# Performance work log

Measured on AMD Instinct MI355X. Metric: run time of the kernel, lower is better.

The kernel has to match this reference:

```python
import jax, jax.numpy as jnp
import numpy as np

B, F, C, O, M = 128, 4096, 32, 32, 9  # batch, num_fields, in_ch, out_ch, num_coeffs (moves incl. self)


def setup_inputs() -> dict:
    key = jax.random.key(0)
    k1, k2, k3, k4 = jax.random.split(key, 4)
    x = jax.random.normal(k1, (B, F, C), dtype=jnp.float32)
    # mask[m, f] = index of the source field feeding target field f via move m
    mask = jax.random.randint(k2, (M, F), 0, F, dtype=jnp.int32)
    init_std = 1.0 / (3.0 * np.sqrt(C * O))  # matches TruncatedNormal stddev in build()
    conv_coeffs = jax.random.normal(k3, (M, C, O), dtype=jnp.float32) * init_std
    # biases are zero-initialized in the original; use small random values so the
    # bias-add path is exercised numerically
    biases = jax.random.normal(k4, (F, O), dtype=jnp.float32) * 0.01
    return {"x": x, "mask": mask, "conv_coeffs": conv_coeffs, "biases": biases}


def reference(x, mask, conv_coeffs, biases):
    # ch_convolve_by_moves: gather source fields per move, per-move matmul, per-field bias.
    # gathered[b, m, f, c] = x[b, mask[m, f], c]
    gathered = jnp.take(x, mask, axis=1)              # [B, M, F, C]
    out = jnp.einsum('bmfc,mco->bfo', gathered, conv_coeffs)  # sum over moves and in-channels
    return out + biases                               # per-field bias broadcast over batch
```

## Files before the change

kernel.cpp:

```cpp
#include <hip/hip_runtime.h>


#define B_ 128
#define F_ 4096
#define C_ 32
#define O_ 32
#define M_ 9
#define T_ 18
#define TF1 32
#define LROW1 528

typedef _Float16 halfx4 __attribute__((ext_vector_type(4)));
typedef _Float16 halfx8 __attribute__((ext_vector_type(8)));
typedef float floatx4 __attribute__((ext_vector_type(4)));
typedef float floatx16 __attribute__((ext_vector_type(16)));

__global__ __launch_bounds__(256) void pass1_transpose(
    const float* __restrict__ x, const float* __restrict__ coeffs,
    _Float16* __restrict__ xh, _Float16* __restrict__ wf)
{
    __shared__ _Float16 tile[TF1 * LROW1];
    const int blk = blockIdx.x;
    const int bs  = blk & 7;
    const int f0  = (blk >> 3) * TF1;
    const int tid = threadIdx.x;

    {
        const int f_l = tid >> 3;
        const int c4  = (tid & 7) * 4;
        const float* src = x + ((size_t)f0 + f_l) * C_ + c4;
#pragma unroll
        for (int bp = 0; bp < 16; ++bp) {
            const floatx4* p = reinterpret_cast<const floatx4*>(
                src + (size_t)(bs * 16 + bp) * (F_ * C_));
            floatx4 v = __builtin_nontemporal_load(p);
            halfx4 hv;
            hv[0] = (_Float16)v[0]; hv[1] = (_Float16)v[1];
            hv[2] = (_Float16)v[2]; hv[3] = (_Float16)v[3];
            *reinterpret_cast<halfx4*>(&tile[f_l * LROW1 + bp * C_ + c4]) = hv;
        }
    }
    __syncthreads();

    {
        const int wv   = tid >> 6;
        const int lane = tid & 63;
#pragma unroll
        for (int it = 0; it < TF1 / 4; ++it) {
            int f_l = it * 4 + wv;
            halfx8 v = *reinterpret_cast<const halfx8*>(&tile[f_l * LROW1 + lane * 8]);
            *reinterpret_cast<halfx8*>(
                xh + ((size_t)bs * F_ + f0 + f_l) * (16 * C_) + lane * 8) = v;
        }
    }

    if (blk == 0) {
        for (int id = tid; id < T_ * 64; id += 256) {
            int t  = id >> 6;
            int L  = id & 63;
            int m  = t >> 1;
            int cb = 16 * (t & 1) + 8 * (L >> 5);
            int o  = L & 31;
            halfx8 w;
#pragma unroll
            for (int j = 0; j < 8; ++j)
                w[j] = (_Float16)coeffs[(m * C_ + cb + j) * O_ + o];
            *reinterpret_cast<halfx8*>(wf + id * 8) = w;
        }
    }
}

__global__ __launch_bounds__(256, 4) void pass2_gemm(
    const _Float16* __restrict__ xh, const _Float16* __restrict__ wf,
    const int* __restrict__ mask, const float* __restrict__ biases,
    float* __restrict__ out)
{
    __shared__ _Float16 sw[T_ * 64 * 8];
    const int tid = threadIdx.x;
#pragma unroll
    for (int i = tid; i < T_ * 64; i += 256)
        reinterpret_cast<halfx8*>(sw)[i] = reinterpret_cast<const halfx8*>(wf)[i];
    __syncthreads();

    const int blk  = blockIdx.x;
    const int bs   = blk & 7;
    const int fg   = blk >> 3;
    const int wave = tid >> 6;
    const int lane = tid & 63;
    const int h    = lane >> 5;
    const int row  = lane & 31;
    const int fi   = row >> 4;
    const int bp   = row & 15;
    const int ocol = lane & 31;

    const int fa = fg * 8 + 2 * wave;
    const int f  = fa + fi;

    const _Float16* xb = xh + (size_t)bs * F_ * (16 * C_) + bp * C_ + 8 * h;

    int sidx[M_];
#pragma unroll
    for (int m = 0; m < M_; ++m) sidx[m] = mask[m * F_ + f];

    halfx8 a[T_];
#pragma unroll
    for (int m = 0; m < M_; ++m) {
        const _Float16* rp = xb + (size_t)sidx[m] * (16 * C_);
        a[2 * m]     = *reinterpret_cast<const halfx8*>(rp);
        a[2 * m + 1] = *reinterpret_cast<const halfx8*>(rp + 16);
    }

    floatx16 acc;
#pragma unroll
    for (int i = 0; i < 16; ++i) acc[i] = 0.0f;
#pragma unroll
    for (int t = 0; t < T_; ++t) {
        halfx8 bwt = *reinterpret_cast<const halfx8*>(&sw[(t * 64 + lane) * 8]);
        acc = __builtin_amdgcn_mfma_f32_32x32x16_f16(a[t], bwt, acc, 0, 0, 0);
    }

    float bias_a = biases[(size_t)fa * O_ + ocol];
    float bias_b = biases[(size_t)(fa + 1) * O_ + ocol];
#pragma unroll
    for (int r = 0; r < 16; ++r) {
        int orow = (r & 3) + 8 * (r >> 2) + 4 * h;
        int ofi  = orow >> 4;
        int b    = bs * 16 + (orow & 15);
        float v  = acc[r] + (ofi ? bias_b : bias_a);
        __builtin_nontemporal_store(
            v, &out[((size_t)b * F_ + fa + ofi) * O_ + ocol]);
    }
}

__global__ __launch_bounds__(256) void fallback_kernel(
    const float* __restrict__ x, const int* __restrict__ mask,
    const float* __restrict__ coeffs, const float* __restrict__ biases,
    float* __restrict__ out)
{
    int gid = blockIdx.x * 256 + threadIdx.x;
    int o = gid & (O_ - 1);
    int f = (gid >> 5) & (F_ - 1);
    int b = gid >> 17;
    float acc = biases[f * O_ + o];
    for (int m = 0; m < M_; ++m) {
        int s = mask[m * F_ + f];
        const float* xr = x + ((size_t)b * F_ + s) * C_;
        const float* wr = coeffs + (m * C_) * O_ + o;
#pragma unroll
        for (int c = 0; c < C_; ++c)
            acc += xr[c] * wr[c * O_];
    }
    out[gid] = acc;
}

extern "C" void kernel_launch(void* const* d_in, const int* in_sizes, int n_in,
                              void* d_out, int out_size, void* d_ws, size_t ws_size,
                              hipStream_t stream) {
    const float* x      = (const float*)d_in[0];
    const int*   mask   = (const int*)d_in[1];
    const float* coeffs = (const float*)d_in[2];
    const float* biases = (const float*)d_in[3];
    float* out = (float*)d_out;

    const size_t xh_elems = (size_t)B_ * F_ * C_;
    const size_t need = xh_elems * sizeof(_Float16) + (size_t)T_ * 64 * 8 * sizeof(_Float16);

    if (ws_size >= need) {
        _Float16* xh = (_Float16*)d_ws;
        _Float16* wf = xh + xh_elems;
        pass1_transpose<<<8 * (F_ / TF1), 256, 0, stream>>>(x, coeffs, xh, wf);
        pass2_gemm<<<8 * (F_ / 8), 256, 0, stream>>>(xh, wf, mask, biases, out);
    } else {
        fallback_kernel<<<(B_ * F_ * O_) / 256, 256, 0, stream>>>(x, mask, coeffs, biases, out);
    }
}
```

Baseline: 143.8 us.

## Fuse fp16 transpose pass into gather-GEMM kernel reading fp32 input directly

Removes the separate transpose/convert pass and workspace. Each block now builds its fp16 weight fragments in shared memory, gathers fp32 rows straight from x, and converts them in registers before the MFMA. The tile shape changes to 4 batches by 8 fields per wave, and block indices are swizzled so that batch groups map across XCDs. This avoids writing and re-reading an fp16 copy of x and saves one launch. In exchange, the gathers fetch twice as many bytes per element, each gathered 128-byte row is only partly used, and every block rebuilds the weights from global memory.

```diff
diff --git a/kernel.cpp b/kernel.cpp
--- a/kernel.cpp
+++ b/kernel.cpp
@@ -7,107 +7,75 @@
 #define O_ 32
 #define M_ 9
 #define T_ 18
-#define TF1 32
-#define LROW1 528
 
-typedef _Float16 halfx4 __attribute__((ext_vector_type(4)));
 typedef _Float16 halfx8 __attribute__((ext_vector_type(8)));
 typedef float floatx4 __attribute__((ext_vector_type(4)));
 typedef float floatx16 __attribute__((ext_vector_type(16)));
 
-__global__ __launch_bounds__(256) void pass1_transpose(
-    const float* __restrict__ x, const float* __restrict__ coeffs,
-    _Float16* __restrict__ xh, _Float16* __restrict__ wf)
+__global__ __launch_bounds__(256, 3) void fused_conv(
+    const float* __restrict__ x, const int* __restrict__ mask,
+    const float* __restrict__ coeffs, const float* __restrict__ biases,
+    float* __restrict__ out)
 {
-    __shared__ _Float16 tile[TF1 * LROW1];
-    const int blk = blockIdx.x;
-    const int bs  = blk & 7;
-    const int f0  = (blk >> 3) * TF1;
+    __shared__ _Float16 sw[T_ * 64 * 8];
+
     const int tid = threadIdx.x;
-
-    {
-        const int f_l = tid >> 3;
-        const int c4  = (tid & 7) * 4;
-        const float* src = x + ((size_t)f0 + f_l) * C_ + c4;
+    for (int id = tid; id < T_ * 64; id += 256) {
+        const int t  = id >> 6;
+        const int L  = id & 63;
+        const int m  = t >> 1;
+        const int cb = 16 * (t & 1) + 8 * (L >> 5);
+        const int oo = L & 31;
+        halfx8 w;
 #pragma unroll
-        for (int bp = 0; bp < 16; ++bp) {
-            const floatx4* p = reinterpret_cast<const floatx4*>(
-                src + (size_t)(bs * 16 + bp) * (F_ * C_));
-            floatx4 v = __builtin_nontemporal_load(p);
-            halfx4 hv;
-            hv[0] = (_Float16)v[0]; hv[1] = (_Float16)v[1];
-            hv[2] = (_Float16)v[2]; hv[3] = (_Float16)v[3];
-            *reinterpret_cast<halfx4*>(&tile[f_l * LROW1 + bp * C_ + c4]) = hv;
-        }
+        for (int jj = 0; jj < 8; ++jj)
+            w[jj] = (_Float16)coeffs[(m * C_ + cb + jj) * O_ + oo];
+        *reinterpret_cast<halfx8*>(&sw[id * 8]) = w;
     }
     __syncthreads();
 
-    {
-        const int wv   = tid >> 6;
-        const int lane = tid & 63;
-#pragma unroll
-        for (int it = 0; it < TF1 / 4; ++it) {
-            int f_l = it * 4 + wv;
-            halfx8 v = *reinterpret_cast<const halfx8*>(&tile[f_l * LROW1 + lane * 8]);
-            *reinterpret_cast<halfx8*>(
-                xh + ((size_t)bs * F_ + f0 + f_l) * (16 * C_) + lane * 8) = v;
-        }
-    }
+    const int blk = blockIdx.x;
+    const int p   = blk >> 10;
+    const int xcd = blk & 7;
+    const int ft  = (blk >> 3) & 127;
+    const int b0  = (p * 8 + xcd) * 4;
+    const int f0  = ft * 32;
 
-    if (blk == 0) {
-        for (int id = tid; id < T_ * 64; id += 256) {
-            int t  = id >> 6;
-            int L  = id & 63;
-            int m  = t >> 1;
-            int cb = 16 * (t & 1) + 8 * (L >> 5);
-            int o  = L & 31;
-            halfx8 w;
-#pragma unroll
-            for (int j = 0; j < 8; ++j)
-                w[j] = (_Float16)coeffs[(m * C_ + cb + j) * O_ + o];
-            *reinterpret_cast<halfx8*>(wf + id * 8) = w;
-        }
-    }
-}
-
-__global__ __launch_bounds__(256, 4) void pass2_gemm(
-    const _Float16* __restrict__ xh, const _Float16* __restrict__ wf,
-    const int* __restrict__ mask, const float* __restrict__ biases,
-    float* __restrict__ out)
-{
-    __shared__ _Float16 sw[T_ * 64 * 8];
-    const int tid = threadIdx.x;
-#pragma unroll
-    for (int i = tid; i < T_ * 64; i += 256)
-        reinterpret_cast<halfx8*>(sw)[i] = reinterpret_cast<const halfx8*>(wf)[i];
-    __syncthreads();
-
-    const int blk  = blockIdx.x;
-    const int bs   = blk & 7;
-    const int fg   = blk >> 3;
     const int wave = tid >> 6;
     const int lane = tid & 63;
     const int h    = lane >> 5;
     const int row  = lane & 31;
-    const int fi   = row >> 4;
-    const int bp   = row & 15;
-    const int ocol = lane & 31;
+    const int fi   = row >> 2;
+    const int bp   = row & 3;
+    const int o    = lane & 31;
 
-    const int fa = fg * 8 + 2 * wave;
-    const int f  = fa + fi;
-
-    const _Float16* xb = xh + (size_t)bs * F_ * (16 * C_) + bp * C_ + 8 * h;
+    const int fw = f0 + wave * 8;
+    const int f  = fw + fi;
 
     int sidx[M_];
 #pragma unroll
     for (int m = 0; m < M_; ++m) sidx[m] = mask[m * F_ + f];
 
+    const float* xrow = x + (size_t)(b0 + bp) * (F_ * C_) + 8 * h;
+
     halfx8 a[T_];
 #pragma unroll
     for (int m = 0; m < M_; ++m) {
-        const _Float16* rp = xb + (size_t)sidx[m] * (16 * C_);
-        a[2 * m]     = *reinterpret_cast<const halfx8*>(rp);
-        a[2 * m + 1] = *reinterpret_cast<const halfx8*>(rp + 16);
+        const float* rp = xrow + (size_t)sidx[m] * C_;
+        const floatx4 v0 = *reinterpret_cast<const floatx4*>(rp);
+        const floatx4 v1 = *reinterpret_cast<const floatx4*>(rp + 4);
+        const floatx4 v2 = *reinterpret_cast<const floatx4*>(rp + 16);
+        const floatx4 v3 = *reinterpret_cast<const floatx4*>(rp + 20);
+        halfx8 lo, hi;
+#pragma unroll
+        for (int jj = 0; jj < 4; ++jj) {
+            lo[jj]     = (_Float16)v0[jj];
+            lo[jj + 4] = (_Float16)v1[jj];
+            hi[jj]     = (_Float16)v2[jj];
+            hi[jj + 4] = (_Float16)v3[jj];
+        }
+        a[2 * m]     = lo;
+        a[2 * m + 1] = hi;
     }
 
     floatx16 acc;
@@ -115,62 +83,30 @@
     for (int i = 0; i < 16; ++i) acc[i] = 0.0f;
 #pragma unroll
     for (int t = 0; t < T_; ++t) {
-        halfx8 bwt = *reinterpret_cast<const halfx8*>(&sw[(t * 64 + lane) * 8]);
+        const halfx8 bwt = *reinterpret_cast<const halfx8*>(&sw[(t * 64 + lane) * 8]);
         acc = __builtin_amdgcn_mfma_f32_32x32x16_f16(a[t], bwt, acc, 0, 0, 0);
     }
 
-    float bias_a = biases[(size_t)fa * O_ + ocol];
-    float bias_b = biases[(size_t)(fa + 1) * O_ + ocol];
+    float bv[4];
+#pragma unroll
+    for (int q = 0; q < 4; ++q)
+        bv[q] = biases[(size_t)(fw + 2 * q + h) * O_ + o];
+
 #pragma unroll
     for (int r = 0; r < 16; ++r) {
-        int orow = (r & 3) + 8 * (r >> 2) + 4 * h;
-        int ofi  = orow >> 4;
-        int b    = bs * 16 + (orow & 15);
-        float v  = acc[r] + (ofi ? bias_b : bias_a);
+        const int q   = r >> 2;
+        const int obp = r & 3;
+        const float v = acc[r] + bv[q];
         __builtin_nontemporal_store(
-            v, &out[((size_t)b * F_ + fa + ofi) * O_ + ocol]);
+            v, &out[((size_t)(b0 + obp) * F_ + fw + 2 * q + h) * O_ + o]);
     }
-}
-
-__global__ __launch_bounds__(256) void fallback_kernel(
-    const float* __restrict__ x, const int* __restrict__ mask,
-    const float* __restrict__ coeffs, const float* __restrict__ biases,
-    float* __restrict__ out)
-{
-    int gid = blockIdx.x * 256 + threadIdx.x;
-    int o = gid & (O_ - 1);
-    int f = (gid >> 5) & (F_ - 1);
-    int b = gid >> 17;
-    float acc = biases[f * O_ + o];
-    for (int m = 0; m < M_; ++m) {
-        int s = mask[m * F_ + f];
-        const float* xr = x + ((size_t)b * F_ + s) * C_;
-        const float* wr = coeffs + (m * C_) * O_ + o;
-#pragma unroll
-        for (int c = 0; c < C_; ++c)
-            acc += xr[c] * wr[c * O_];
-    }
-    out[gid] = acc;
 }
 
 extern "C" void kernel_launch(void* const* d_in, const int* in_sizes, int n_in,
                               void* d_out, int out_size, void* d_ws, size_t ws_size,
                               hipStream_t stream) {
-    const float* x      = (const float*)d_in[0];
-    const int*   mask   = (const int*)d_in[1];
-    const float* coeffs = (const float*)d_in[2];
-    const float* biases = (const float*)d_in[3];
-    float* out = (float*)d_out;
-
-    const size_t xh_elems = (size_t)B_ * F_ * C_;
-    const size_t need = xh_elems * sizeof(_Float16) + (size_t)T_ * 64 * 8 * sizeof(_Float16);
-
-    if (ws_size >= need) {
-        _Float16* xh = (_Float16*)d_ws;
-        _Float16* wf = xh + xh_elems;
-        pass1_transpose<<<8 * (F_ / TF1), 256, 0, stream>>>(x, coeffs, xh, wf);
-        pass2_gemm<<<8 * (F_ / 8), 256, 0, stream>>>(xh, wf, mask, biases, out);
-    } else {
-        fallback_kernel<<<(B_ * F_ * O_) / 256, 256, 0, stream>>>(x, mask, coeffs, biases, out);
-    }
+    (void)in_sizes; (void)n_in; (void)d_ws; (void)ws_size; (void)out_size;
+    fused_conv<<<4 * 8 * 128, 256, 0, stream>>>(
+        (const float*)d_in[0], (const int*)d_in[1],
+        (const float*)d_in[2], (const float*)d_in[3], (float*)d_out);
 }
```

Result: slower. 176.1 us (+22.4%).
